# Optimization experiments

Measured on AMD Instinct MI355X. Metric: run time of the kernel, lower is better.

The kernel has to match this reference:

```python
import jax, jax.numpy as jnp
import numpy as np

N, E, F_IN, EDGE_DIM, EMB, H, L, DENSE = 50000, 800000, 16, 4, 32, 4, 2, 128
HC = EMB * H


def setup_inputs() -> dict:
    ks = iter(jax.random.split(jax.random.key(0), 64))

    def w(shape, fan):
        return jax.random.normal(next(ks), shape, jnp.float32) / np.float32(np.sqrt(fan))

    inp = {}
    inp['x'] = jax.random.normal(next(ks), (N, F_IN), jnp.float32)
    inp['edge_index'] = jax.random.randint(next(ks), (2, E), 0, N, jnp.int32)
    inp['edge_attr'] = jax.random.normal(next(ks), (E, EDGE_DIM), jnp.float32)
    # layer-0 TransformerConv (F_IN -> EMB, H heads) + transf Linear
    inp['Wq0'] = w((F_IN, HC), F_IN); inp['bq0'] = w((HC,), HC)
    inp['Wk0'] = w((F_IN, HC), F_IN); inp['bk0'] = w((HC,), HC)
    inp['Wv0'] = w((F_IN, HC), F_IN); inp['bv0'] = w((HC,), HC)
    inp['We0'] = w((EDGE_DIM, HC), EDGE_DIM)
    inp['Ws0'] = w((F_IN, HC), F_IN); inp['bs0'] = w((HC,), HC)
    inp['Wt0'] = w((HC, EMB), HC); inp['bt0'] = w((EMB,), EMB)
    # stacked L inner layers (EMB -> EMB)
    inp['Wq'] = w((L, EMB, HC), EMB); inp['bq'] = w((L, HC), HC)
    inp['Wk'] = w((L, EMB, HC), EMB); inp['bk'] = w((L, HC), HC)
    inp['Wv'] = w((L, EMB, HC), EMB); inp['bv'] = w((L, HC), HC)
    inp['We'] = w((L, EDGE_DIM, HC), EDGE_DIM)
    inp['Ws'] = w((L, EMB, HC), EMB); inp['bs'] = w((L, HC), HC)
    inp['Wt'] = w((L, HC, EMB), HC); inp['bt'] = w((L, EMB), EMB)
    # dense head
    inp['W1'] = w((EMB, DENSE), EMB); inp['b1'] = w((DENSE,), DENSE)
    inp['W2'] = w((DENSE, DENSE // 2), DENSE); inp['b2'] = w((DENSE // 2,), DENSE)
    inp['W3'] = w((DENSE // 2, 1), DENSE // 2); inp['b3'] = w((1,), 1)
    return inp


def _tconv(h, edge_attr, src, dst, Wq, bq, Wk, bk, Wv, bv, We, Ws, bs):
    """PyG TransformerConv: edge-conditioned multi-head attention + root skip."""
    n = h.shape[0]
    q = (h @ Wq + bq).reshape(n, H, EMB)
    k = (h @ Wk + bk).reshape(n, H, EMB)
    v = (h @ Wv + bv).reshape(n, H, EMB)
    e = (edge_attr @ We).reshape(-1, H, EMB)          # [E,H,C]
    kj = k[src] + e                                   # gather + edge bias
    logits = (q[dst] * kj).sum(-1) / np.float32(np.sqrt(EMB))  # [E,H]
    m = jax.ops.segment_max(logits, dst, num_segments=n)       # segment softmax
    p = jnp.exp(logits - m[dst])
    z = jax.ops.segment_sum(p, dst, num_segments=n)
    alpha = p / (z[dst] + 1e-16)
    msg = (v[src] + e) * alpha[:, :, None]
    out = jax.ops.segment_sum(msg, dst, num_segments=n).reshape(n, HC)
    return out + h @ Ws + bs                          # root_weight skip


def _forward(x, edge_attr, Wq0, bq0, Wk0, bk0, Wv0, bv0, We0, Ws0, bs0, Wt0, bt0,
             Wq, bq, Wk, bk, Wv, bv, We, Ws, bs, Wt, bt,
             W1, b1, W2, b2, W3, b3, edge_index):
    src, dst = edge_index[0], edge_index[1]
    h = _tconv(x, edge_attr, src, dst, Wq0, bq0, Wk0, bk0, Wv0, bv0, We0, Ws0, bs0)
    h = jax.nn.relu(h @ Wt0 + bt0)
    for i in range(L):
        h = _tconv(h, edge_attr, src, dst, Wq[i], bq[i], Wk[i], bk[i],
                   Wv[i], bv[i], We[i], Ws[i], bs[i])
        h = jax.nn.relu(h @ Wt[i] + bt[i])
    h = jax.nn.relu(h @ W1 + b1)
    h = jax.nn.relu(h @ W2 + b2)
    return jax.nn.sigmoid(h @ W3 + b3)                # [N,1]


def reference(x, edge_index, edge_attr, Wq0, bq0, Wk0, bk0, Wv0, bv0, We0, Ws0, bs0,
              Wt0, bt0, Wq, bq, Wk, bk, Wv, bv, We, Ws, bs, Wt, bt,
              W1, b1, W2, b2, W3, b3):
    return _forward(x, edge_attr, Wq0, bq0, Wk0, bk0, Wv0, bv0, We0, Ws0, bs0,
                    Wt0, bt0, Wq, bq, Wk, bk, Wv, bv, We, Ws, bs, Wt, bt,
                    W1, b1, W2, b2, W3, b3, edge_index)
```

## Files before the change

### kernel.cpp

```cpp
#include <hip/hip_runtime.h>

#define NN 50000
#define EE 800000
#define FIN 16
#define EDIM 4
#define EMB 32
#define NH 4
#define HC 128
#define NL 2
#define DENSE 128
#define QNPB 50
#define SBLK 49

typedef _Float16 h2 __attribute__((ext_vector_type(2)));
union HU { unsigned int u; h2 h; };

__device__ __forceinline__ h2 u2h(unsigned int u) { HU c; c.u = u; return c.h; }
__device__ __forceinline__ unsigned int h2u(h2 h) { HU c; c.h = h; return c.u; }

#if defined(__has_builtin)
#  if __has_builtin(__builtin_amdgcn_fdot2)
#    define FDOT2(a, b, c) __builtin_amdgcn_fdot2((a), (b), (c), false)
#  endif
#endif
#ifndef FDOT2
__device__ __forceinline__ float fdot2_sw(h2 a, h2 b, float c) {
    return fmaf((float)a.x, (float)b.x, fmaf((float)a.y, (float)b.y, c));
}
#  define FDOT2(a, b, c) fdot2_sw((a), (b), (c))
#endif

__device__ __forceinline__ float2 h2f2(unsigned int u) {
    union { unsigned int u; _Float16 h[2]; } c; c.u = u;
    return make_float2((float)c.h[0], (float)c.h[1]);
}
__device__ __forceinline__ unsigned int pkh2(float a, float b) {
    union { unsigned int u; _Float16 h[2]; } c;
    c.h[0] = (_Float16)a; c.h[1] = (_Float16)b; return c.u;
}

__global__ void hist_kernel(const int* __restrict__ dst, int* __restrict__ counts) {
    int e = blockIdx.x * blockDim.x + threadIdx.x;
    if (e < EE) atomicAdd(&counts[dst[e]], 1);
}

__global__ __launch_bounds__(1024) void scan1_kernel(const int* __restrict__ cursor,
                                                     int* __restrict__ row_ptr,
                                                     int* __restrict__ bsum) {
    __shared__ int wsum[16];
    __shared__ int wpre[17];
    int tid = threadIdx.x, lane = tid & 63, wid = tid >> 6;
    int i = blockIdx.x * 1024 + tid;
    int v = (i < NN) ? cursor[i] : 0;
    int incl = v;
    #pragma unroll
    for (int off = 1; off < 64; off <<= 1) {
        int t = __shfl_up(incl, off, 64);
        if (lane >= off) incl += t;
    }
    if (lane == 63) wsum[wid] = incl;
    __syncthreads();
    if (tid == 0) {
        int acc = 0;
        #pragma unroll
        for (int w = 0; w < 16; ++w) { wpre[w] = acc; acc += wsum[w]; }
        wpre[16] = acc;
    }
    __syncthreads();
    if (i < NN) row_ptr[i] = wpre[wid] + incl - v;
    if (tid == 0) bsum[blockIdx.x] = wpre[16];
}

__global__ __launch_bounds__(1024) void scan3_kernel(int* __restrict__ row_ptr,
                                                     int* __restrict__ cursor,
                                                     const int* __restrict__ bsum) {
    __shared__ int boff_s;
    __shared__ int total_s;
    int tid = threadIdx.x;
    if (tid < 64) {
        int v = (tid < SBLK) ? bsum[tid] : 0;
        int incl = v;
        #pragma unroll
        for (int off = 1; off < 64; off <<= 1) {
            int u = __shfl_up(incl, off, 64);
            if (tid >= off) incl += u;
        }
        if (tid == (int)blockIdx.x) boff_s = incl - v;
        if (tid == 63) total_s = incl;
    }
    __syncthreads();
    int i = blockIdx.x * 1024 + tid;
    if (i < NN) {
        int r = row_ptr[i] + boff_s;
        row_ptr[i] = r;
        cursor[i] = r;
    }
    if (blockIdx.x == 0 && tid == 0) row_ptr[NN] = total_s;
}

__global__ void scatter_kernel(const int* __restrict__ src, const int* __restrict__ dst,
                               const float* __restrict__ ea, int* __restrict__ cursor,
                               uint4* __restrict__ edges) {
    int e = blockIdx.x * blockDim.x + threadIdx.x;
    if (e >= EE) return;
    int d = dst[e];
    int pos = atomicAdd(&cursor[d], 1);
    float4 q = *reinterpret_cast<const float4*>(ea + (size_t)e * 4);
    uint4 rec;
    rec.x = (unsigned int)src[e];
    rec.y = pkh2(q.x, q.y);
    rec.z = pkh2(q.z, q.w);
    rec.w = 0u;
    edges[pos] = rec;
}

__global__ __launch_bounds__(512) void qkvs0_kernel(const float* __restrict__ x,
        const float* __restrict__ Wq, const float* __restrict__ bq,
        const float* __restrict__ Wk, const float* __restrict__ bk,
        const float* __restrict__ Wv, const float* __restrict__ bv,
        const float* __restrict__ Ws, const float* __restrict__ bs,
        _Float16* __restrict__ Qh, _Float16* __restrict__ kvh,
        float* __restrict__ Out) {
    __shared__ __align__(16) float hs[QNPB * FIN];
    int tid = threadIdx.x;
    int m = tid >> 7, c = tid & 127;
    const float* W; const float* b;
    switch (m) {
        case 0:  W = Wq; b = bq; break;
        case 1:  W = Wk; b = bk; break;
        case 2:  W = Wv; b = bv; break;
        default: W = Ws; b = bs; break;
    }
    float w[FIN];
    #pragma unroll
    for (int f = 0; f < FIN; ++f) w[f] = W[f * HC + c];
    float bias = b[c];
    int node0 = blockIdx.x * QNPB;
    {
        const float4* src4 = (const float4*)(x + (size_t)node0 * FIN);
        float4* dst4 = (float4*)hs;
        for (int i = tid; i < QNPB * FIN / 4; i += 512) dst4[i] = src4[i];
    }
    __syncthreads();
    const float4* hs4 = (const float4*)hs;
    int kvi = ((c >> 1) << 2) + (c & 1);
    for (int k = 0; k < QNPB; ++k) {
        float s = bias;
        #pragma unroll
        for (int f4 = 0; f4 < FIN / 4; ++f4) {
            float4 hv = hs4[k * (FIN / 4) + f4];
            s += hv.x * w[4 * f4] + hv.y * w[4 * f4 + 1]
               + hv.z * w[4 * f4 + 2] + hv.w * w[4 * f4 + 3];
        }
        size_t n = node0 + k;
        if      (m == 0) Qh[n * HC + c] = (_Float16)s;
        else if (m == 1) kvh[n * 256 + kvi] = (_Float16)s;
        else if (m == 2) kvh[n * 256 + kvi + 2] = (_Float16)s;
        else             Out[n * HC + c] = s;
    }
}

__global__ __launch_bounds__(512) void ftq_kernel(const float* __restrict__ Wt,
        const float* __restrict__ bt,
        const float* __restrict__ Wq, const float* __restrict__ bq,
        const float* __restrict__ Wk, const float* __restrict__ bk,
        const float* __restrict__ Wv, const float* __restrict__ bv,
        const float* __restrict__ Ws, const float* __restrict__ bs,
        _Float16* __restrict__ Qh, _Float16* __restrict__ kvh,
        float* __restrict__ Out) {
    __shared__ __align__(16) float os[QNPB * HC];
    __shared__ __align__(16) float hs[QNPB * EMB];
    int tid = threadIdx.x;
    int node0 = blockIdx.x * QNPB;
    int g = tid >> 7;

    {
        const float4* src4 = (const float4*)(Out + (size_t)node0 * HC);
        float4* dst4 = (float4*)os;
        for (int i = tid; i < QNPB * HC / 4; i += 512) dst4[i] = src4[i];
    }

    int cT = (tid & 127) >> 2, seg = tid & 3;
    float wt[32];
    #pragma unroll
    for (int j = 0; j < 32; ++j) wt[j] = Wt[(seg * 32 + j) * EMB + cT];
    float btc = bt[cT];
    __syncthreads();
    for (int k = g; k < QNPB; k += 4) {
        float p = 0.f;
        const float4* r4 = (const float4*)(os + k * HC + seg * 32);
        #pragma unroll
        for (int j4 = 0; j4 < 8; ++j4) {
            float4 rv = r4[j4];
            p += rv.x * wt[4 * j4] + rv.y * wt[4 * j4 + 1]
               + rv.z * wt[4 * j4 + 2] + rv.w * wt[4 * j4 + 3];
        }
        p += __shfl_xor(p, 1, 64);
        p += __shfl_xor(p, 2, 64);
        if (seg == 0) hs[k * EMB + cT] = fmaxf(p + btc, 0.f);
    }
    __syncthreads();

    int m = tid >> 7, c = tid & 127;
    const float* W; const float* b;
    switch (m) {
        case 0:  W = Wq; b = bq; break;
        case 1:  W = Wk; b = bk; break;
        case 2:  W = Wv; b = bv; break;
        default: W = Ws; b = bs; break;
    }
    float w[EMB];
    #pragma unroll
    for (int f = 0; f < EMB; ++f) w[f] = W[f * HC + c];
    float bias = b[c];
    const float4* hs4 = (const float4*)hs;
    int kvi = ((c >> 1) << 2) + (c & 1);
    for (int k = 0; k < QNPB; ++k) {
        float s = bias;
        #pragma unroll
        for (int f4 = 0; f4 < EMB / 4; ++f4) {
            float4 hv = hs4[k * (EMB / 4) + f4];
            s += hv.x * w[4 * f4] + hv.y * w[4 * f4 + 1]
               + hv.z * w[4 * f4 + 2] + hv.w * w[4 * f4 + 3];
        }
        size_t n = node0 + k;
        if      (m == 0) Qh[n * HC + c] = (_Float16)s;
        else if (m == 1) kvh[n * 256 + kvi] = (_Float16)s;
        else if (m == 2) kvh[n * 256 + kvi + 2] = (_Float16)s;
        else             Out[n * HC + c] = s;
    }
}

__global__ __launch_bounds__(256) void edge_attn_kernel(const int* __restrict__ row_ptr,
        const uint4* __restrict__ edges,
        const float* __restrict__ We,
        const unsigned int* __restrict__ Qp, const uint2* __restrict__ kvp,
        float2* __restrict__ Out) {
    int n = blockIdx.x * 4 + (threadIdx.x >> 6);
    int lane = threadIdx.x & 63;
    int c0 = 2 * lane, c1 = 2 * lane + 1;
    h2 w01_0 = { (_Float16)We[0 * HC + c0], (_Float16)We[1 * HC + c0] };
    h2 w23_0 = { (_Float16)We[2 * HC + c0], (_Float16)We[3 * HC + c0] };
    h2 w01_1 = { (_Float16)We[0 * HC + c1], (_Float16)We[1 * HC + c1] };
    h2 w23_1 = { (_Float16)We[2 * HC + c1], (_Float16)We[3 * HC + c1] };
    h2 q = u2h(Qp[(size_t)n * 64 + lane]);
    int start = row_ptr[n], end = row_ptr[n + 1];
    float z = 0.f, acc0 = 0.f, acc1 = 0.f;
    const float SC = 0.17677669529663687f;
    const char* kvb = (const char*)kvp;
    unsigned int loff = (unsigned int)lane << 3;
    int i = start;
    for (; i + 1 < end; i += 2) {
        uint4 rA = edges[i], rB = edges[i + 1];
        uint2 kvA = *(const uint2*)(kvb + ((rA.x << 9) + loff));
        uint2 kvB = *(const uint2*)(kvb + ((rB.x << 9) + loff));
        h2 eaA01 = u2h(rA.y), eaA23 = u2h(rA.z);
        h2 eaB01 = u2h(rB.y), eaB23 = u2h(rB.z);
        float eA0 = FDOT2(eaA01, w01_0, FDOT2(eaA23, w23_0, 0.f));
        float eA1 = FDOT2(eaA01, w01_1, FDOT2(eaA23, w23_1, 0.f));
        float eB0 = FDOT2(eaB01, w01_0, FDOT2(eaB23, w23_0, 0.f));
        float eB1 = FDOT2(eaB01, w01_1, FDOT2(eaB23, w23_1, 0.f));
        h2 eApk = { (_Float16)eA0, (_Float16)eA1 };
        h2 eBpk = { (_Float16)eB0, (_Float16)eB1 };
        h2 kA = u2h(kvA.x), vA = u2h(kvA.y);
        h2 kB = u2h(kvB.x), vB = u2h(kvB.y);
        float pA = FDOT2(q, kA + eApk, 0.f);
        float pB = FDOT2(q, kB + eBpk, 0.f);
        #pragma unroll
        for (int off = 1; off < 16; off <<= 1) {
            pA += __shfl_xor(pA, off, 64);
            pB += __shfl_xor(pB, off, 64);
        }
        float xA = __expf(pA * SC), xB = __expf(pB * SC);
        z += xA + xB;
        h2 veA = vA + eApk, veB = vB + eBpk;
        float2 vfA = h2f2(h2u(veA)), vfB = h2f2(h2u(veB));
        acc0 += xA * vfA.x + xB * vfB.x;
        acc1 += xA * vfA.y + xB * vfB.y;
    }
    if (i < end) {
        uint4 r = edges[i];
        uint2 kv = *(const uint2*)(kvb + ((r.x << 9) + loff));
        h2 ea01 = u2h(r.y), ea23 = u2h(r.z);
        float e0 = FDOT2(ea01, w01_0, FDOT2(ea23, w23_0, 0.f));
        float e1 = FDOT2(ea01, w01_1, FDOT2(ea23, w23_1, 0.f));
        h2 epk = { (_Float16)e0, (_Float16)e1 };
        h2 k = u2h(kv.x), v = u2h(kv.y);
        float p = FDOT2(q, k + epk, 0.f);
        #pragma unroll
        for (int off = 1; off < 16; off <<= 1) p += __shfl_xor(p, off, 64);
        float x = __expf(p * SC);
        z += x;
        h2 ve = v + epk;
        float2 vf = h2f2(h2u(ve));
        acc0 += x * vf.x;
        acc1 += x * vf.y;
    }
    float inv = 1.f / (z + 1e-16f);
    size_t oi = (size_t)n * 64 + lane;
    float2 o = Out[oi];
    o.x += acc0 * inv;
    o.y += acc1 * inv;
    Out[oi] = o;
}

__global__ __launch_bounds__(512) void head2_kernel(const float* __restrict__ Outb,
        const float* __restrict__ Wt, const float* __restrict__ bt,
        const float* __restrict__ W1, const float* __restrict__ b1,
        const float* __restrict__ W2, const float* __restrict__ b2,
        const float* __restrict__ W3, const float* __restrict__ b3,
        float* __restrict__ out) {
    __shared__ __align__(16) float os[QNPB * HC];
    __shared__ __align__(16) float hs[QNPB * EMB];
    __shared__ __align__(16) float d2s[QNPB * 64];
    float* d1s = os;
    int tid = threadIdx.x;
    int node0 = blockIdx.x * QNPB;
    int g = tid >> 7;

    {
        const float4* src4 = (const float4*)(Outb + (size_t)node0 * HC);
        float4* dst4 = (float4*)os;
        for (int i = tid; i < QNPB * HC / 4; i += 512) dst4[i] = src4[i];
    }

    int cT = (tid & 127) >> 2, seg = tid & 3;
    float wt[32];
    #pragma unroll
    for (int j = 0; j < 32; ++j) wt[j] = Wt[(seg * 32 + j) * EMB + cT];
    float btc = bt[cT];
    __syncthreads();
    for (int k = g; k < QNPB; k += 4) {
        float p = 0.f;
        const float4* r4 = (const float4*)(os + k * HC + seg * 32);
        #pragma unroll
        for (int j4 = 0; j4 < 8; ++j4) {
            float4 rv = r4[j4];
            p += rv.x * wt[4 * j4] + rv.y * wt[4 * j4 + 1]
               + rv.z * wt[4 * j4 + 2] + rv.w * wt[4 * j4 + 3];
        }
        p += __shfl_xor(p, 1, 64);
        p += __shfl_xor(p, 2, 64);
        if (seg == 0) hs[k * EMB + cT] = fmaxf(p + btc, 0.f);
    }
    __syncthreads();

    int c1 = tid & 127;
    float w1[32];
    #pragma unroll
    for (int f = 0; f < 32; ++f) w1[f] = W1[f * DENSE + c1];
    float b1c = b1[c1];
    const float4* hs4 = (const float4*)hs;
    for (int k = g; k < QNPB; k += 4) {
        float s = b1c;
        #pragma unroll
        for (int f4 = 0; f4 < 8; ++f4) {
            float4 hv = hs4[k * 8 + f4];
            s += hv.x * w1[4 * f4] + hv.y * w1[4 * f4 + 1]
               + hv.z * w1[4 * f4 + 2] + hv.w * w1[4 * f4 + 3];
        }
        d1s[k * DENSE + c1] = fmaxf(s, 0.f);
    }
    __syncthreads();

    int c2 = (tid & 127) >> 1, hh = tid & 1;
    float w2[64];
    #pragma unroll
    for (int j = 0; j < 64; ++j) w2[j] = W2[(hh * 64 + j) * 64 + c2];
    float b2c = b2[c2];
    for (int k = g; k < QNPB; k += 4) {
        float p = 0.f;
        const float4* r4 = (const float4*)(d1s + k * DENSE + hh * 64);
        #pragma unroll
        for (int j4 = 0; j4 < 16; ++j4) {
            float4 rv = r4[j4];
            p += rv.x * w2[4 * j4] + rv.y * w2[4 * j4 + 1]
               + rv.z * w2[4 * j4 + 2] + rv.w * w2[4 * j4 + 3];
        }
        p += __shfl_xor(p, 1, 64);
        if (hh == 0) d2s[k * 64 + c2] = fmaxf(p + b2c, 0.f);
    }
    __syncthreads();

    int w = tid >> 6, lane = tid & 63;
    float w3r = W3[lane];
    float b3r = b3[0];
    for (int k = w; k < QNPB; k += 8) {
        float t = d2s[k * 64 + lane] * w3r;
        #pragma unroll
        for (int off = 1; off < 64; off <<= 1) t += __shfl_xor(t, off, 64);
        if (lane == 0) out[node0 + k] = 1.f / (1.f + __expf(-(t + b3r)));
    }
}

extern "C" void kernel_launch(void* const* d_in, const int* in_sizes, int n_in,
                              void* d_out, int out_size, void* d_ws, size_t ws_size,
                              hipStream_t stream) {
    const float* x   = (const float*)d_in[0];
    const int*   ei  = (const int*)d_in[1];
    const float* ea  = (const float*)d_in[2];
    const float* Wq0 = (const float*)d_in[3];  const float* bq0 = (const float*)d_in[4];
    const float* Wk0 = (const float*)d_in[5];  const float* bk0 = (const float*)d_in[6];
    const float* Wv0 = (const float*)d_in[7];  const float* bv0 = (const float*)d_in[8];
    const float* We0 = (const float*)d_in[9];
    const float* Ws0 = (const float*)d_in[10]; const float* bs0 = (const float*)d_in[11];
    const float* Wt0 = (const float*)d_in[12]; const float* bt0 = (const float*)d_in[13];
    const float* WqL = (const float*)d_in[14]; const float* bqL = (const float*)d_in[15];
    const float* WkL = (const float*)d_in[16]; const float* bkL = (const float*)d_in[17];
    const float* WvL = (const float*)d_in[18]; const float* bvL = (const float*)d_in[19];
    const float* WeL = (const float*)d_in[20];
    const float* WsL = (const float*)d_in[21]; const float* bsL = (const float*)d_in[22];
    const float* WtL = (const float*)d_in[23]; const float* btL = (const float*)d_in[24];
    const float* W1  = (const float*)d_in[25]; const float* b1  = (const float*)d_in[26];
    const float* W2  = (const float*)d_in[27]; const float* b2  = (const float*)d_in[28];
    const float* W3  = (const float*)d_in[29]; const float* b3  = (const float*)d_in[30];
    float* out = (float*)d_out;

    char* ws = (char*)d_ws;
    size_t off = 0;
    auto alloc = [&](size_t bytes) -> void* {
        void* p = ws + off; off = (off + bytes + 255) & ~(size_t)255; return p;
    };
    int*      cursor  = (int*)     alloc((size_t)NN * 4);
    int*      row_ptr = (int*)     alloc((size_t)(NN + 1) * 4);
    int*      bsum    = (int*)     alloc((size_t)SBLK * 4);
    uint4*    edges   = (uint4*)   alloc((size_t)EE * 16);
    _Float16* Qh      = (_Float16*)alloc((size_t)NN * HC * 2);
    _Float16* kvh     = (_Float16*)alloc((size_t)NN * HC * 2 * 2);
    float*    Outb    = (float*)   alloc((size_t)NN * HC * 4);

    hipMemsetAsync(cursor, 0, (size_t)NN * 4, stream);
    hist_kernel<<<(EE + 255) / 256, 256, 0, stream>>>(ei + EE, cursor);
    scan1_kernel<<<SBLK, 1024, 0, stream>>>(cursor, row_ptr, bsum);
    scan3_kernel<<<SBLK, 1024, 0, stream>>>(row_ptr, cursor, bsum);
    scatter_kernel<<<(EE + 255) / 256, 256, 0, stream>>>(ei, ei + EE, ea, cursor, edges);

    const uint2* kvp = (const uint2*)kvh;
    const unsigned int* Qp = (const unsigned int*)Qh;
    float2* Out2 = (float2*)Outb;

    qkvs0_kernel<<<NN / QNPB, 512, 0, stream>>>(x, Wq0, bq0, Wk0, bk0, Wv0, bv0,
                                                Ws0, bs0, Qh, kvh, Outb);
    edge_attn_kernel<<<NN / 4, 256, 0, stream>>>(row_ptr, edges, We0, Qp, kvp, Out2);

    ftq_kernel<<<NN / QNPB, 512, 0, stream>>>(Wt0, bt0,
        WqL, bqL, WkL, bkL, WvL, bvL, WsL, bsL, Qh, kvh, Outb);
    edge_attn_kernel<<<NN / 4, 256, 0, stream>>>(row_ptr, edges, WeL, Qp, kvp, Out2);

    ftq_kernel<<<NN / QNPB, 512, 0, stream>>>(WtL, btL,
        WqL + EMB * HC, bqL + HC, WkL + EMB * HC, bkL + HC,
        WvL + EMB * HC, bvL + HC, WsL + EMB * HC, bsL + HC, Qh, kvh, Outb);
    edge_attn_kernel<<<NN / 4, 256, 0, stream>>>(row_ptr, edges,
        WeL + EDIM * HC, Qp, kvp, Out2);

    head2_kernel<<<NN / QNPB, 512, 0, stream>>>(Outb, WtL + (size_t)HC * EMB, btL + EMB,
                                                W1, b1, W2, b2, W3, b3, out);
}
```

Before: 626.5 us.

## Split each wave into two half-waves processing alternate edges with 4 channels per lane

```diff
diff --git a/kernel.cpp b/kernel.cpp
--- a/kernel.cpp
+++ b/kernel.cpp
@@ -234,74 +234,81 @@
 __global__ __launch_bounds__(256) void edge_attn_kernel(const int* __restrict__ row_ptr,
         const uint4* __restrict__ edges,
         const float* __restrict__ We,
-        const unsigned int* __restrict__ Qp, const uint2* __restrict__ kvp,
-        float2* __restrict__ Out) {
+        const uint2* __restrict__ Qp, const uint4* __restrict__ kvp,
+        float4* __restrict__ Out) {
     int n = blockIdx.x * 4 + (threadIdx.x >> 6);
     int lane = threadIdx.x & 63;
-    int c0 = 2 * lane, c1 = 2 * lane + 1;
-    h2 w01_0 = { (_Float16)We[0 * HC + c0], (_Float16)We[1 * HC + c0] };
-    h2 w23_0 = { (_Float16)We[2 * HC + c0], (_Float16)We[3 * HC + c0] };
-    h2 w01_1 = { (_Float16)We[0 * HC + c1], (_Float16)We[1 * HC + c1] };
-    h2 w23_1 = { (_Float16)We[2 * HC + c1], (_Float16)We[3 * HC + c1] };
-    h2 q = u2h(Qp[(size_t)n * 64 + lane]);
+    int half = lane >> 5, sl = lane & 31;
+    h2 w01[4], w23[4];
+    #pragma unroll
+    for (int j = 0; j < 4; ++j) {
+        int c = 4 * sl + j;
+        w01[j] = (h2){ (_Float16)We[c],          (_Float16)We[HC + c] };
+        w23[j] = (h2){ (_Float16)We[2 * HC + c], (_Float16)We[3 * HC + c] };
+    }
+    uint2 qw = Qp[(size_t)n * 32 + sl];
+    h2 q01 = u2h(qw.x), q23 = u2h(qw.y);
     int start = row_ptr[n], end = row_ptr[n + 1];
-    float z = 0.f, acc0 = 0.f, acc1 = 0.f;
+    float z = 0.f, a0 = 0.f, a1 = 0.f, a2 = 0.f, a3 = 0.f;
     const float SC = 0.17677669529663687f;
     const char* kvb = (const char*)kvp;
-    unsigned int loff = (unsigned int)lane << 3;
-    int i = start;
-    for (; i + 1 < end; i += 2) {
-        uint4 rA = edges[i], rB = edges[i + 1];
-        uint2 kvA = *(const uint2*)(kvb + ((rA.x << 9) + loff));
-        uint2 kvB = *(const uint2*)(kvb + ((rB.x << 9) + loff));
-        h2 eaA01 = u2h(rA.y), eaA23 = u2h(rA.z);
-        h2 eaB01 = u2h(rB.y), eaB23 = u2h(rB.z);
-        float eA0 = FDOT2(eaA01, w01_0, FDOT2(eaA23, w23_0, 0.f));
-        float eA1 = FDOT2(eaA01, w01_1, FDOT2(eaA23, w23_1, 0.f));
-        float eB0 = FDOT2(eaB01, w01_0, FDOT2(eaB23, w23_0, 0.f));
-        float eB1 = FDOT2(eaB01, w01_1, FDOT2(eaB23, w23_1, 0.f));
-        h2 eApk = { (_Float16)eA0, (_Float16)eA1 };
-        h2 eBpk = { (_Float16)eB0, (_Float16)eB1 };
-        h2 kA = u2h(kvA.x), vA = u2h(kvA.y);
-        h2 kB = u2h(kvB.x), vB = u2h(kvB.y);
-        float pA = FDOT2(q, kA + eApk, 0.f);
-        float pB = FDOT2(q, kB + eBpk, 0.f);
-        #pragma unroll
-        for (int off = 1; off < 16; off <<= 1) {
-            pA += __shfl_xor(pA, off, 64);
-            pB += __shfl_xor(pB, off, 64);
-        }
-        float xA = __expf(pA * SC), xB = __expf(pB * SC);
-        z += xA + xB;
-        h2 veA = vA + eApk, veB = vB + eBpk;
-        float2 vfA = h2f2(h2u(veA)), vfB = h2f2(h2u(veB));
-        acc0 += xA * vfA.x + xB * vfB.x;
-        acc1 += xA * vfA.y + xB * vfB.y;
-    }
-    if (i < end) {
-        uint4 r = edges[i];
-        uint2 kv = *(const uint2*)(kvb + ((r.x << 9) + loff));
-        h2 ea01 = u2h(r.y), ea23 = u2h(r.z);
-        float e0 = FDOT2(ea01, w01_0, FDOT2(ea23, w23_0, 0.f));
-        float e1 = FDOT2(ea01, w01_1, FDOT2(ea23, w23_1, 0.f));
-        h2 epk = { (_Float16)e0, (_Float16)e1 };
-        h2 k = u2h(kv.x), v = u2h(kv.y);
-        float p = FDOT2(q, k + epk, 0.f);
-        #pragma unroll
-        for (int off = 1; off < 16; off <<= 1) p += __shfl_xor(p, off, 64);
-        float x = __expf(p * SC);
-        z += x;
-        h2 ve = v + epk;
-        float2 vf = h2f2(h2u(ve));
-        acc0 += x * vf.x;
-        acc1 += x * vf.y;
-    }
-    float inv = 1.f / (z + 1e-16f);
-    size_t oi = (size_t)n * 64 + lane;
-    float2 o = Out[oi];
-    o.x += acc0 * inv;
-    o.y += acc1 * inv;
-    Out[oi] = o;
+    unsigned int loff = (unsigned int)sl << 4;
+    for (int i = start; i < end; i += 8) {
+        uint4 rec[4], kv[4];
+        bool val[4];
+        #pragma unroll
+        for (int u = 0; u < 4; ++u) {
+            int e = i + 2 * u + half;
+            val[u] = e < end;
+            int le = val[u] ? e : end - 1;
+            rec[u] = edges[le];
+        }
+        #pragma unroll
+        for (int u = 0; u < 4; ++u)
+            kv[u] = *(const uint4*)(kvb + ((rec[u].x << 9) + loff));
+        float p[4]; h2 ep01[4], ep23[4];
+        #pragma unroll
+        for (int u = 0; u < 4; ++u) {
+            h2 ea01 = u2h(rec[u].y), ea23 = u2h(rec[u].z);
+            float e0 = FDOT2(ea01, w01[0], FDOT2(ea23, w23[0], 0.f));
+            float e1 = FDOT2(ea01, w01[1], FDOT2(ea23, w23[1], 0.f));
+            float e2 = FDOT2(ea01, w01[2], FDOT2(ea23, w23[2], 0.f));
+            float e3 = FDOT2(ea01, w01[3], FDOT2(ea23, w23[3], 0.f));
+            ep01[u] = (h2){ (_Float16)e0, (_Float16)e1 };
+            ep23[u] = (h2){ (_Float16)e2, (_Float16)e3 };
+            p[u] = FDOT2(q01, u2h(kv[u].x) + ep01[u],
+                   FDOT2(q23, u2h(kv[u].z) + ep23[u], 0.f));
+        }
+        #pragma unroll
+        for (int off = 1; off < 8; off <<= 1) {
+            #pragma unroll
+            for (int u = 0; u < 4; ++u) p[u] += __shfl_xor(p[u], off, 64);
+        }
+        #pragma unroll
+        for (int u = 0; u < 4; ++u) {
+            float x = __expf(p[u] * SC);
+            x = val[u] ? x : 0.f;
+            z += x;
+            h2 v01 = u2h(kv[u].y) + ep01[u], v23 = u2h(kv[u].w) + ep23[u];
+            float2 f01 = h2f2(h2u(v01)), f23 = h2f2(h2u(v23));
+            a0 += x * f01.x; a1 += x * f01.y; a2 += x * f23.x; a3 += x * f23.y;
+        }
+    }
+    z  += __shfl_xor(z, 32, 64);
+    a0 += __shfl_xor(a0, 32, 64);
+    a1 += __shfl_xor(a1, 32, 64);
+    a2 += __shfl_xor(a2, 32, 64);
+    a3 += __shfl_xor(a3, 32, 64);
+    if (half == 0) {
+        float inv = 1.f / (z + 1e-16f);
+        size_t oi = (size_t)n * 32 + sl;
+        float4 o = Out[oi];
+        o.x += a0 * inv;
+        o.y += a1 * inv;
+        o.z += a2 * inv;
+        o.w += a3 * inv;
+        Out[oi] = o;
+    }
 }
 
 __global__ __launch_bounds__(512) void head2_kernel(const float* __restrict__ Outb,
@@ -435,23 +442,23 @@
     scan3_kernel<<<SBLK, 1024, 0, stream>>>(row_ptr, cursor, bsum);
     scatter_kernel<<<(EE + 255) / 256, 256, 0, stream>>>(ei, ei + EE, ea, cursor, edges);
 
-    const uint2* kvp = (const uint2*)kvh;
-    const unsigned int* Qp = (const unsigned int*)Qh;
-    float2* Out2 = (float2*)Outb;
+    const uint4* kvp4 = (const uint4*)kvh;
+    const uint2* Qp2 = (const uint2*)Qh;
+    float4* Out4 = (float4*)Outb;
 
     qkvs0_kernel<<<NN / QNPB, 512, 0, stream>>>(x, Wq0, bq0, Wk0, bk0, Wv0, bv0,
                                                 Ws0, bs0, Qh, kvh, Outb);
-    edge_attn_kernel<<<NN / 4, 256, 0, stream>>>(row_ptr, edges, We0, Qp, kvp, Out2);
+    edge_attn_kernel<<<NN / 4, 256, 0, stream>>>(row_ptr, edges, We0, Qp2, kvp4, Out4);
 
     ftq_kernel<<<NN / QNPB, 512, 0, stream>>>(Wt0, bt0,
         WqL, bqL, WkL, bkL, WvL, bvL, WsL, bsL, Qh, kvh, Outb);
-    edge_attn_kernel<<<NN / 4, 256, 0, stream>>>(row_ptr, edges, WeL, Qp, kvp, Out2);
+    edge_attn_kernel<<<NN / 4, 256, 0, stream>>>(row_ptr, edges, WeL, Qp2, kvp4, Out4);
 
     ftq_kernel<<<NN / QNPB, 512, 0, stream>>>(WtL, btL,
         WqL + EMB * HC, bqL + HC, WkL + EMB * HC, bkL + HC,
         WvL + EMB * HC, bvL + HC, WsL + EMB * HC, bsL + HC, Qh, kvh, Outb);
     edge_attn_kernel<<<NN / 4, 256, 0, stream>>>(row_ptr, edges,
-        WeL + EDIM * HC, Qp, kvp, Out2);
+        WeL + EDIM * HC, Qp2, kvp4, Out4);
 
     head2_kernel<<<NN / QNPB, 512, 0, stream>>>(Outb, WtL + (size_t)HC * EMB, btL + EMB,
                                                 W1, b1, W2, b2, W3, b3, out);
```

Result: faster. 585.5 us (-6.6%).
